# Kernel optimization log

Hardware: AMD Instinct MI355X
Metric: run time of the kernel (lower is better)

## Reference

```python
import jax, jax.numpy as jnp
import numpy as np

B = 16384
A_SCALE = 1.7159
S_SCALE = 2.0 / 3.0
CONNECTIONS = [[0,1,2],[1,2,3],[2,3,4],[3,4,5],[0,4,5],[0,1,5],
               [0,1,2,3],[1,2,3,4],[2,3,4,5],[0,3,4,5],[0,1,4,5],[0,1,2,5],
               [0,1,3,4],[1,2,4,5],[0,2,3,5],[0,1,2,3,4,5]]

def _c3_mask():
    m = np.zeros((16, 6, 1, 1), dtype=np.float32)
    for i, conns in enumerate(CONNECTIONS):
        m[i, conns, 0, 0] = 1.0
    return jnp.asarray(m)

C3_MASK = _c3_mask()

def tanh_act(x):
    return A_SCALE * jnp.tanh(S_SCALE * x)

def conv_valid(x, w):
    # x: (B, Cin, H, W), w: (Cout, Cin, k, k) -> (B, Cout, H-k+1, W-k+1)
    return jax.lax.conv_general_dilated(
        x, w, window_strides=(1, 1), padding='VALID',
        dimension_numbers=('NCHW', 'OIHW', 'NCHW'))

def pool_affine(x, w, b):
    # Faithful to the torch 'efficient' path: reshape(B,C,H/2,W/2,2,2).mean((4,5)).
    # (This is a row-major regrouping, NOT true 2x2 block pooling.)
    bsz, c, h, wd = x.shape
    y = x.reshape(bsz, c, h // 2, wd // 2, 2, 2).mean(axis=(4, 5))
    return w.reshape(1, c, 1, 1) * y + b.reshape(1, c, 1, 1)


def setup_inputs() -> dict:
    key = jax.random.key(0)
    ks = jax.random.split(key, 14)
    inp = {
        'x':     jax.random.normal(ks[0], (B, 1, 32, 32), jnp.float32),
        'w1':    jax.random.normal(ks[1], (6, 1, 5, 5), jnp.float32) * 0.2,
        'b1':    jnp.zeros((6,), jnp.float32),
        's2_w':  jnp.ones((6,), jnp.float32),
        's2_b':  jnp.zeros((6,), jnp.float32),
        'w3':    jax.random.normal(ks[2], (16, 6, 5, 5), jnp.float32) * 0.1,
        'b3':    jnp.zeros((16,), jnp.float32),
        's4_w':  jnp.ones((16,), jnp.float32),
        's4_b':  jnp.zeros((16,), jnp.float32),
        'w5':    jax.random.normal(ks[3], (120, 16, 5, 5), jnp.float32) * 0.05,
        'b5':    jnp.zeros((120,), jnp.float32),
        'f6_w':  jax.random.normal(ks[4], (84, 120), jnp.float32) * 0.09,
        'f6_b':  jnp.zeros((84,), jnp.float32),
        'rbf_w': jax.random.bernoulli(ks[5], 0.3, (10, 84)).astype(jnp.float32),
    }
    return inp


def reference(x, w1, b1, s2_w, s2_b, w3, b3, s4_w, s4_b, w5, b5, f6_w, f6_b, rbf_w):
    # C1: full conv 1->6, per-filter scalar bias
    h = conv_valid(x, w1) + b1.reshape(1, -1, 1, 1)          # (B,6,28,28)
    h = tanh_act(h)
    # S2: avg pool (efficient reshape semantics) + learnable affine
    h = tanh_act(pool_affine(h, s2_w, s2_b))                  # (B,6,14,14)
    # C3: sparsely-connected conv 6->16, implemented as masked full conv
    h = conv_valid(h, w3 * C3_MASK) + b3.reshape(1, -1, 1, 1)  # (B,16,10,10)
    h = tanh_act(h)
    # S4
    h = tanh_act(pool_affine(h, s4_w, s4_b))                  # (B,16,5,5)
    # C5: full conv 16->120 on 5x5 -> 1x1, squeeze to (B,120)
    h = conv_valid(h, w5) + b5.reshape(1, -1, 1, 1)
    h = tanh_act(h.reshape(h.shape[0], 120))                  # (B,120)
    # F6
    h = tanh_act(h @ f6_w.T + f6_b)                           # (B,84)
    # RBF: squared euclidean distance to each class bitmap
    diff = h[:, None, :] - rbf_w[None, :, :]                  # (B,10,84)
    return jnp.sum(diff * diff, axis=2)                       # (B,10)
```

## Files before the change

### kernel.cpp

```cpp
#include <hip/hip_runtime.h>
#include <cstdint>


typedef unsigned int u32;

union U32H2 { u32 u; _Float16 h[2]; };
__device__ __forceinline__ float f16lo(u32 v) { U32H2 a; a.u = v; return (float)a.h[0]; }
__device__ __forceinline__ float f16hi(u32 v) { U32H2 a; a.u = v; return (float)a.h[1]; }
__device__ __forceinline__ u32 packh2(float a, float b) {
    U32H2 x; x.h[0] = (_Float16)a; x.h[1] = (_Float16)b; return x.u;
}

typedef _Float16 h2v __attribute__((ext_vector_type(2)));
union U32V2 { u32 u; h2v v; };

#if defined(__has_builtin)
#if __has_builtin(__builtin_amdgcn_fdot2)
#define HAVE_FDOT2 1
#endif
#endif

__device__ __forceinline__ float dot2(u32 a, u32 b, float c) {
    U32V2 x, y; x.u = a; y.u = b;
#ifdef HAVE_FDOT2
    return __builtin_amdgcn_fdot2(x.v, y.v, c, false);
#else
    return c + (float)x.v[0] * (float)y.v[0] + (float)x.v[1] * (float)y.v[1];
#endif
}

__device__ __forceinline__ float tact(float v) {
    float e = __expf(1.3333333333f * v);
    return 1.7159f * (1.0f - 2.0f * __builtin_amdgcn_rcpf(e + 1.0f));
}

__device__ const int C3_NIC[16] = {3,3,3,3,3,3, 4,4,4,4,4,4,4,4,4, 6};
__device__ const int C3_ICL[96] = {
    0,1,2,0,0,0,  1,2,3,0,0,0,  2,3,4,0,0,0,  3,4,5,0,0,0,
    0,4,5,0,0,0,  0,1,5,0,0,0,  0,1,2,3,0,0,  1,2,3,4,0,0,
    2,3,4,5,0,0,  0,3,4,5,0,0,  0,1,4,5,0,0,  0,1,2,5,0,0,
    0,1,3,4,0,0,  1,2,4,5,0,0,  0,2,3,5,0,0,  0,1,2,3,4,5 };

#define WPK_W1  0
#define WPK_W1S 96
#define WPK_W3  192
#define WPK_W3S 1632
#define WPK_W5  3072
#define WPK_F6  31872
#define WPK_N   36912

__global__ __launch_bounds__(256) void k_wpack(
    const float* __restrict__ w1, const float* __restrict__ w3,
    const float* __restrict__ w5, const float* __restrict__ f6w,
    u32* __restrict__ wpk)
{
    const int idx = blockIdx.x * 256 + threadIdx.x;
    if (idx >= WPK_N) return;
    float a = 0.0f, b = 0.0f;
    if (idx < 192) {
        const int s = idx >= 96;
        const int t = idx - s * 96;
        if (t < 90) {
            int ch = t / 15, r = t % 15, ky = r / 3, q = r % 3;
            const float* w = w1 + ch * 25 + ky * 5;
            if (!s) { a = w[2 * q]; if (q < 2) b = w[2 * q + 1]; }
            else if (q == 0) { b = w[0]; }
            else { a = w[2 * q - 1]; b = w[2 * q]; }
        }
    } else if (idx < WPK_W5) {
        const int s = (idx - WPK_W3) >= 1440;
        const int t = idx - WPK_W3 - s * 1440;
        int p = t / 15, r = t % 15, ky = r / 3, q = r % 3;
        const float* w = w3 + p * 25 + ky * 5;
        if (!s) { a = w[2 * q]; if (q < 2) b = w[2 * q + 1]; }
        else if (q == 0) { b = w[0]; }
        else { a = w[2 * q - 1]; b = w[2 * q]; }
    } else if (idx < WPK_F6) {
        int t = idx - WPK_W5;
        int c = t / 240, r = t % 240, g = r / 3, q = r % 3;
        a = w5[c * 400 + g * 5 + 2 * q];
        if (q < 2) b = w5[c * 400 + g * 5 + 2 * q + 1];
    } else {
        int t = idx - WPK_F6;
        int o = t / 60, i = t % 60;
        a = f6w[o * 120 + 2 * i];
        b = f6w[o * 120 + 2 * i + 1];
    }
    wpk[idx] = packh2(a, b);
}

__global__ __launch_bounds__(256) void k_tr(const float* __restrict__ x,
                                            u32* __restrict__ xp)
{
    __shared__ _Float16 lds[64 * 66];
    const int t = threadIdx.x;
    const int tb = blockIdx.x * 64;
    const int tp = blockIdx.y * 64;
    #pragma unroll
    for (int i = 0; i < 16; ++i) {
        int idx = i * 256 + t;
        int bl = idx >> 6, pl = idx & 63;
        lds[pl * 66 + bl] = (_Float16)x[(size_t)(tb + bl) * 1024 + tp + pl];
    }
    __syncthreads();
    #pragma unroll
    for (int j = 0; j < 8; ++j) {
        int idx = j * 256 + t;
        int pp = idx >> 6, bl = idx & 63;
        U32H2 u;
        u.h[0] = lds[(2 * pp) * 66 + bl];
        u.h[1] = lds[(2 * pp + 1) * 66 + bl];
        xp[(size_t)(blockIdx.y * 32 + pp) * 8192 + tb + bl] = u.u;
    }
}

__global__ __launch_bounds__(256) void k_c1s2(
    const u32* __restrict__ xp, const u32* __restrict__ wpk,
    const float* __restrict__ b1,
    const float* __restrict__ s2w, const float* __restrict__ s2b,
    u32* __restrict__ s2p, int ostr)
{
    const int sl = blockIdx.x * 256 + threadIdx.x;
    const int oy2 = blockIdx.y / 3;
    const int cp  = blockIdx.y % 3;
    const int y0 = 2 * oy2;
    const u32* xb = xp + sl;

    u32 wl[2][15], wls[2][15];
    #pragma unroll
    for (int a = 0; a < 2; ++a) {
        #pragma unroll
        for (int i = 0; i < 15; ++i) wl[a][i]  = wpk[WPK_W1  + (2 * cp + a) * 15 + i];
        #pragma unroll
        for (int i = 0; i < 15; ++i) wls[a][i] = wpk[WPK_W1S + (2 * cp + a) * 15 + i];
    }

    u32 cur[6][4];
    #pragma unroll
    for (int r = 0; r < 6; ++r)
        #pragma unroll
        for (int c = 0; c < 4; ++c)
            cur[r][c] = xb[(size_t)((y0 + r) * 16 + c) * 8192];

    float va[2][7], vb[2][7];

    #pragma unroll
    for (int qx = 0; qx < 7; ++qx) {
        float o[2][2][4];
        #pragma unroll
        for (int a = 0; a < 2; ++a) {
            const float bbv = b1[2 * cp + a];
            #pragma unroll
            for (int u = 0; u < 2; ++u)
                #pragma unroll
                for (int d = 0; d < 4; ++d) o[a][u][d] = bbv;
        }
        #pragma unroll
        for (int r = 0; r < 6; ++r) {
            #pragma unroll
            for (int u = 0; u < 2; ++u) {
                const int ky = r - u;
                if (ky < 0 || ky > 4) continue;
                #pragma unroll
                for (int a = 0; a < 2; ++a) {
                    const u32 w0 = wl[a][ky * 3 + 0];
                    const u32 w1 = wl[a][ky * 3 + 1];
                    const u32 w2 = wl[a][ky * 3 + 2];
                    const u32 v0 = wls[a][ky * 3 + 0];
                    const u32 v1 = wls[a][ky * 3 + 1];
                    const u32 v2 = wls[a][ky * 3 + 2];
                    o[a][u][0] = dot2(cur[r][0], w0, dot2(cur[r][1], w1, dot2(cur[r][2], w2, o[a][u][0])));
                    o[a][u][1] = dot2(cur[r][0], v0, dot2(cur[r][1], v1, dot2(cur[r][2], v2, o[a][u][1])));
                    o[a][u][2] = dot2(cur[r][1], w0, dot2(cur[r][2], w1, dot2(cur[r][3], w2, o[a][u][2])));
                    o[a][u][3] = dot2(cur[r][1], v0, dot2(cur[r][2], v1, dot2(cur[r][3], v2, o[a][u][3])));
                }
            }
        }
        #pragma unroll
        for (int a = 0; a < 2; ++a) {
            const int ch = 2 * cp + a;
            const float sw = s2w[ch], sb = s2b[ch];
            float m0 = 0.25f * (tact(o[a][0][0]) + tact(o[a][0][1]) + tact(o[a][0][2]) + tact(o[a][0][3]));
            float m1 = 0.25f * (tact(o[a][1][0]) + tact(o[a][1][1]) + tact(o[a][1][2]) + tact(o[a][1][3]));
            va[a][qx] = tact(sw * m0 + sb);
            vb[a][qx] = tact(sw * m1 + sb);
        }
        if (qx < 6) {
            #pragma unroll
            for (int r = 0; r < 6; ++r) {
                cur[r][0] = cur[r][2];
                cur[r][1] = cur[r][3];
                cur[r][2] = xb[(size_t)((y0 + r) * 16 + 2 * qx + 4) * 8192];
                cur[r][3] = xb[(size_t)((y0 + r) * 16 + 2 * qx + 5) * 8192];
            }
        }
    }
    #pragma unroll
    for (int a = 0; a < 2; ++a) {
        u32 o7[7];
        o7[0] = packh2(va[a][0], va[a][1]);
        o7[1] = packh2(va[a][2], va[a][3]);
        o7[2] = packh2(va[a][4], va[a][5]);
        o7[3] = packh2(va[a][6], vb[a][0]);
        o7[4] = packh2(vb[a][1], vb[a][2]);
        o7[5] = packh2(vb[a][3], vb[a][4]);
        o7[6] = packh2(vb[a][5], vb[a][6]);
        const int ch = 2 * cp + a;
        const int f0 = ch * 98 + oy2 * 7;
        const int fh0 = f0 >> 1;
        uint2* p2 = (uint2*)s2p;
        uint2 t;
        if ((oy2 & 1) == 0) {
            t.x = o7[0]; t.y = o7[1]; p2[(size_t)(fh0 + 0) * ostr + sl] = t;
            t.x = o7[2]; t.y = o7[3]; p2[(size_t)(fh0 + 1) * ostr + sl] = t;
            t.x = o7[4]; t.y = o7[5]; p2[(size_t)(fh0 + 2) * ostr + sl] = t;
            s2p[((size_t)(fh0 + 3) * ostr + sl) * 2] = o7[6];
        } else {
            s2p[((size_t)fh0 * ostr + sl) * 2 + 1] = o7[0];
            t.x = o7[1]; t.y = o7[2]; p2[(size_t)(fh0 + 1) * ostr + sl] = t;
            t.x = o7[3]; t.y = o7[4]; p2[(size_t)(fh0 + 2) * ostr + sl] = t;
            t.x = o7[5]; t.y = o7[6]; p2[(size_t)(fh0 + 3) * ostr + sl] = t;
        }
    }
}

template<int NIC>
__device__ __forceinline__ void c3_body(
    const uint2* __restrict__ s2c, const u32* __restrict__ wpk,
    const int* __restrict__ icl, int oc, int y2, int nb, int sl,
    float a2[2][10])
{
    #pragma unroll
    for (int e = 0; e < NIC; ++e) {
        const int ic = icl[e];
        const uint2* sp = s2c + (size_t)(ic * 49 + y2 * 7) * nb + sl;
        u32 wa_[6][7];
        #pragma unroll
        for (int k = 0; k < 21; ++k) {
            const uint2 v = sp[(size_t)k * nb];
            wa_[(2 * k) / 7][(2 * k) % 7]         = v.x;
            wa_[(2 * k + 1) / 7][(2 * k + 1) % 7] = v.y;
        }
        u32 wl[15], wls[15];
        #pragma unroll
        for (int i = 0; i < 15; ++i) wl[i]  = wpk[WPK_W3  + (oc * 6 + ic) * 15 + i];
        #pragma unroll
        for (int i = 0; i < 15; ++i) wls[i] = wpk[WPK_W3S + (oc * 6 + ic) * 15 + i];
        #pragma unroll
        for (int r = 0; r < 6; ++r) {
            const u32* wa = wa_[r];
            #pragma unroll
            for (int u = 0; u < 2; ++u) {
                const int ky = r - u;
                if (ky < 0 || ky > 4) continue;
                const u32 w0 = wl[ky * 3 + 0];
                const u32 w1 = wl[ky * 3 + 1];
                const u32 w2 = wl[ky * 3 + 2];
                const u32 v0 = wls[ky * 3 + 0];
                const u32 v1 = wls[ky * 3 + 1];
                const u32 v2 = wls[ky * 3 + 2];
                #pragma unroll
                for (int p = 0; p < 5; ++p) {
                    a2[u][2 * p]     = dot2(wa[p], w0, dot2(wa[p + 1], w1, dot2(wa[p + 2], w2, a2[u][2 * p])));
                    a2[u][2 * p + 1] = dot2(wa[p], v0, dot2(wa[p + 1], v1, dot2(wa[p + 2], v2, a2[u][2 * p + 1])));
                }
            }
        }
    }
}

__global__ __launch_bounds__(256) void k_c3s4(
    const u32* __restrict__ s2p, const u32* __restrict__ wpk,
    const float* __restrict__ b3, const float* __restrict__ s4w,
    const float* __restrict__ s4b, u32* __restrict__ s4p, int nb)
{
    const int sl = blockIdx.x * 256 + threadIdx.x;
    const int oc = blockIdx.y / 5;
    const int y2 = blockIdx.y % 5;
    const uint2* s2c = (const uint2*)s2p;
    const int* icl = &C3_ICL[oc * 6];
    const float bbv = b3[oc];

    float a2[2][10];
    #pragma unroll
    for (int u = 0; u < 2; ++u)
        #pragma unroll
        for (int ox = 0; ox < 10; ++ox) a2[u][ox] = bbv;

    switch (C3_NIC[oc]) {
        case 3:  c3_body<3>(s2c, wpk, icl, oc, y2, nb, sl, a2); break;
        case 4:  c3_body<4>(s2c, wpk, icl, oc, y2, nb, sl, a2); break;
        default: c3_body<6>(s2c, wpk, icl, oc, y2, nb, sl, a2); break;
    }

    float tv[20];
    #pragma unroll
    for (int u = 0; u < 2; ++u)
        #pragma unroll
        for (int ox = 0; ox < 10; ++ox) tv[u * 10 + ox] = tact(a2[u][ox]);
    const float swv = s4w[oc], sbv = s4b[oc];
    float so[5];
    #pragma unroll
    for (int x2 = 0; x2 < 5; ++x2)
        so[x2] = tact(0.25f * (tv[x2 * 4] + tv[x2 * 4 + 1] + tv[x2 * 4 + 2] + tv[x2 * 4 + 3]) * swv + sbv);
    const size_t g = (size_t)(oc * 5 + y2) * 3;
    s4p[(g + 0) * nb + sl] = packh2(so[0], so[1]);
    s4p[(g + 1) * nb + sl] = packh2(so[2], so[3]);
    s4p[(g + 2) * nb + sl] = packh2(so[4], 0.0f);
}

__global__ __launch_bounds__(256) void k_c5(
    const u32* __restrict__ s4p, const u32* __restrict__ wpk,
    const float* __restrict__ b5, u32* __restrict__ h5p, int nb)
{
    const int sl = blockIdx.x * 256 + threadIdx.x;
    const int chg = blockIdx.y;
    const u32* wp = wpk + WPK_W5 + chg * 10 * 240;
    float acc[10];
    #pragma unroll
    for (int c = 0; c < 10; ++c) acc[c] = b5[chg * 10 + c];
    #pragma unroll 4
    for (int i = 0; i < 240; ++i) {
        const u32 v = s4p[(size_t)i * nb + sl];
        #pragma unroll
        for (int c = 0; c < 10; ++c)
            acc[c] = dot2(v, wp[c * 240 + i], acc[c]);
    }
    #pragma unroll
    for (int j = 0; j < 5; ++j)
        h5p[(size_t)(chg * 5 + j) * nb + sl] =
            packh2(tact(acc[2 * j]), tact(acc[2 * j + 1]));
}

__global__ __launch_bounds__(256) void k_f6(
    const u32* __restrict__ h5p, const u32* __restrict__ wpk,
    const float* __restrict__ f6b, u32* __restrict__ h6p, int nb)
{
    const int sl = blockIdx.x * 256 + threadIdx.x;
    const int og = blockIdx.y;
    const u32* wp = wpk + WPK_F6 + og * 14 * 60;
    float acc[14];
    #pragma unroll
    for (int o = 0; o < 14; ++o) acc[o] = f6b[og * 14 + o];
    #pragma unroll 4
    for (int i = 0; i < 60; ++i) {
        const u32 v = h5p[(size_t)i * nb + sl];
        #pragma unroll
        for (int o = 0; o < 14; ++o)
            acc[o] = dot2(v, wp[o * 60 + i], acc[o]);
    }
    #pragma unroll
    for (int j = 0; j < 7; ++j)
        h6p[(size_t)(og * 7 + j) * nb + sl] =
            packh2(tact(acc[2 * j]), tact(acc[2 * j + 1]));
}

__global__ __launch_bounds__(256) void k_rbf(
    const u32* __restrict__ h6p, const float* __restrict__ rbf,
    float* __restrict__ out, int nb)
{
    const int sl = blockIdx.x * 256 + threadIdx.x;
    const int gy = blockIdx.y;
    float hv[84];
    #pragma unroll
    for (int i = 0; i < 42; ++i) {
        const u32 v = h6p[(size_t)i * nb + sl];
        hv[2 * i]     = f16lo(v);
        hv[2 * i + 1] = f16hi(v);
    }
    #pragma unroll
    for (int a = 0; a < 2; ++a) {
        const int c = 2 * gy + a;
        float acc = 0.0f;
        #pragma unroll 4
        for (int i = 0; i < 84; ++i) {
            float d = hv[i] - rbf[c * 84 + i];
            acc += d * d;
        }
        out[(size_t)sl * 10 + c] = acc;
    }
}

extern "C" void kernel_launch(void* const* d_in, const int* in_sizes, int n_in,
                              void* d_out, int out_size, void* d_ws, size_t ws_size,
                              hipStream_t stream)
{
    const float* x    = (const float*)d_in[0];
    const float* w1   = (const float*)d_in[1];
    const float* b1   = (const float*)d_in[2];
    const float* s2w  = (const float*)d_in[3];
    const float* s2b  = (const float*)d_in[4];
    const float* w3   = (const float*)d_in[5];
    const float* b3   = (const float*)d_in[6];
    const float* s4w  = (const float*)d_in[7];
    const float* s4b  = (const float*)d_in[8];
    const float* w5   = (const float*)d_in[9];
    const float* b5   = (const float*)d_in[10];
    const float* f6w  = (const float*)d_in[11];
    const float* f6b  = (const float*)d_in[12];
    const float* rbfw = (const float*)d_in[13];
    float* out = (float*)d_out;
    char* ws = (char*)d_ws;

    u32* WPK = (u32*)((char*)d_out +
                      (((size_t)out_size - (size_t)(WPK_N * 4)) & ~(size_t)7));
    k_wpack<<<dim3((WPK_N + 255) / 256), 256, 0, stream>>>(w1, w3, w5, f6w, WPK);

    if (ws_size >= 55312384) {
        u32* S2P = (u32*)(ws);
        u32* XP  = (u32*)(ws + 38535168);
        u32* S4P = (u32*)(ws + 38535168);
        u32* H5P = (u32*)(ws);
        u32* H6P = (u32*)(ws + 4194304);
        for (int c = 0; c < 2; ++c) {
            k_tr  <<<dim3(128, 16), 256, 0, stream>>>(x + (size_t)c * 8192 * 1024, XP);
            k_c1s2<<<dim3(32, 42), 256, 0, stream>>>(XP, WPK, b1, s2w, s2b,
                                                     S2P + (size_t)c * 16384, 16384);
        }
        k_c3s4<<<dim3(64, 80), 256, 0, stream>>>(S2P, WPK, b3, s4w, s4b, S4P, 16384);
        k_c5  <<<dim3(64, 12), 256, 0, stream>>>(S4P, WPK, b5, H5P, 16384);
        k_f6  <<<dim3(64, 6), 256, 0, stream>>>(H5P, WPK, f6b, H6P, 16384);
        k_rbf <<<dim3(64, 5), 256, 0, stream>>>(H6P, rbfw, out, 16384);
    } else {
        u32* XP  = (u32*)(ws);
        u32* S2P = (u32*)(ws + 16777216);
        u32* S4P = (u32*)(ws);
        u32* H5P = (u32*)(ws + 7864320);
        u32* H6P = (u32*)(ws + 9830400);
        for (int c = 0; c < 2; ++c) {
            k_tr  <<<dim3(128, 16), 256, 0, stream>>>(x + (size_t)c * 8192 * 1024, XP);
            k_c1s2<<<dim3(32, 42), 256, 0, stream>>>(XP, WPK, b1, s2w, s2b, S2P, 8192);
            k_c3s4<<<dim3(32, 80), 256, 0, stream>>>(S2P, WPK, b3, s4w, s4b, S4P, 8192);
            k_c5  <<<dim3(32, 12), 256, 0, stream>>>(S4P, WPK, b5, H5P, 8192);
            k_f6  <<<dim3(32, 6), 256, 0, stream>>>(H5P, WPK, f6b, H6P, 8192);
            k_rbf <<<dim3(32, 5), 256, 0, stream>>>(H6P, rbfw, out + (size_t)c * 8192 * 10, 8192);
        }
    }
}
```

Before: 321.5 us.

## Widen intermediate layouts to 8-byte loads and split C3 into two row halves

All intermediate activation buffers (transposed input, S4, H5, H6) switch from one packed half2 per batch element to uint2 pairs, so each thread issues 8-byte loads and stores. The C3/S4 kernel now computes three or two pooled output rows per block instead of one. This lets a thread reuse one loaded slab of S2 rows across several rows and cuts redundant S2 reads, reducing the grid from 80 to 32 blocks in y. The trade-off is more accumulators and registers per thread, which may lower occupancy, and uneven work between the two halves.

```diff
diff --git a/kernel.cpp b/kernel.cpp
--- a/kernel.cpp
+++ b/kernel.cpp
@@ -104,13 +104,16 @@
     }
     __syncthreads();
     #pragma unroll
-    for (int j = 0; j < 8; ++j) {
+    for (int j = 0; j < 4; ++j) {
         int idx = j * 256 + t;
-        int pp = idx >> 6, bl = idx & 63;
-        U32H2 u;
-        u.h[0] = lds[(2 * pp) * 66 + bl];
-        u.h[1] = lds[(2 * pp + 1) * 66 + bl];
-        xp[(size_t)(blockIdx.y * 32 + pp) * 8192 + tb + bl] = u.u;
+        int pc = idx >> 6, bl = idx & 63;
+        U32H2 u0, u1;
+        u0.h[0] = lds[(4 * pc + 0) * 66 + bl];
+        u0.h[1] = lds[(4 * pc + 1) * 66 + bl];
+        u1.h[0] = lds[(4 * pc + 2) * 66 + bl];
+        u1.h[1] = lds[(4 * pc + 3) * 66 + bl];
+        uint2 o; o.x = u0.u; o.y = u1.u;
+        ((uint2*)xp)[(size_t)(blockIdx.y * 16 + pc) * 8192 + tb + bl] = o;
     }
 }
 
@@ -124,7 +127,7 @@
     const int oy2 = blockIdx.y / 3;
     const int cp  = blockIdx.y % 3;
     const int y0 = 2 * oy2;
-    const u32* xb = xp + sl;
+    const uint2* xb = (const uint2*)xp + sl;
 
     u32 wl[2][15], wls[2][15];
     #pragma unroll
@@ -137,10 +140,13 @@
 
     u32 cur[6][4];
     #pragma unroll
-    for (int r = 0; r < 6; ++r)
-        #pragma unroll
-        for (int c = 0; c < 4; ++c)
-            cur[r][c] = xb[(size_t)((y0 + r) * 16 + c) * 8192];
+    for (int r = 0; r < 6; ++r) {
+        #pragma unroll
+        for (int cc = 0; cc < 2; ++cc) {
+            const uint2 v = xb[(size_t)((y0 + r) * 8 + cc) * 8192];
+            cur[r][2 * cc] = v.x; cur[r][2 * cc + 1] = v.y;
+        }
+    }
 
     float va[2][7], vb[2][7];
 
@@ -188,10 +194,11 @@
         if (qx < 6) {
             #pragma unroll
             for (int r = 0; r < 6; ++r) {
+                const uint2 v = xb[(size_t)((y0 + r) * 8 + qx + 2) * 8192];
                 cur[r][0] = cur[r][2];
                 cur[r][1] = cur[r][3];
-                cur[r][2] = xb[(size_t)((y0 + r) * 16 + 2 * qx + 4) * 8192];
-                cur[r][3] = xb[(size_t)((y0 + r) * 16 + 2 * qx + 5) * 8192];
+                cur[r][2] = v.x;
+                cur[r][3] = v.y;
             }
         }
     }
@@ -224,22 +231,44 @@
     }
 }
 
-template<int NIC>
-__device__ __forceinline__ void c3_body(
+__device__ __forceinline__ void emit_s4(
+    const float a2[2][10], int oc, int y2, float swv, float sbv,
+    u32* __restrict__ s4p, int nb, int sl)
+{
+    float tv[20];
+    #pragma unroll
+    for (int u = 0; u < 2; ++u)
+        #pragma unroll
+        for (int ox = 0; ox < 10; ++ox) tv[u * 10 + ox] = tact(a2[u][ox]);
+    float so[5];
+    #pragma unroll
+    for (int x2 = 0; x2 < 5; ++x2)
+        so[x2] = tact(0.25f * (tv[x2 * 4] + tv[x2 * 4 + 1] + tv[x2 * 4 + 2] + tv[x2 * 4 + 3]) * swv + sbv);
+    const int g0 = (oc * 5 + y2) * 3;
+    #pragma unroll
+    for (int q = 0; q < 3; ++q) {
+        const int g = g0 + q;
+        const float lo = (q < 2) ? so[2 * q] : so[4];
+        const float hi = (q < 2) ? so[2 * q + 1] : 0.0f;
+        s4p[((size_t)(g >> 1) * nb + sl) * 2 + (g & 1)] = packh2(lo, hi);
+    }
+}
+
+template<int NIC, int Y2_0, int NY2, int R0, int NCELL>
+__device__ __forceinline__ void c3_half(
     const uint2* __restrict__ s2c, const u32* __restrict__ wpk,
-    const int* __restrict__ icl, int oc, int y2, int nb, int sl,
-    float a2[2][10])
+    const int* __restrict__ icl, int oc, int nb, int sl,
+    float a2[NY2][2][10])
 {
     #pragma unroll
     for (int e = 0; e < NIC; ++e) {
         const int ic = icl[e];
-        const uint2* sp = s2c + (size_t)(ic * 49 + y2 * 7) * nb + sl;
-        u32 wa_[6][7];
-        #pragma unroll
-        for (int k = 0; k < 21; ++k) {
+        const uint2* sp = s2c + (size_t)(ic * 49 + (R0 * 7) / 2) * nb + sl;
+        u32 wf[NCELL * 2];
+        #pragma unroll
+        for (int k = 0; k < NCELL; ++k) {
             const uint2 v = sp[(size_t)k * nb];
-            wa_[(2 * k) / 7][(2 * k) % 7]         = v.x;
-            wa_[(2 * k + 1) / 7][(2 * k + 1) % 7] = v.y;
+            wf[2 * k] = v.x; wf[2 * k + 1] = v.y;
         }
         u32 wl[15], wls[15];
         #pragma unroll
@@ -247,22 +276,25 @@
         #pragma unroll
         for (int i = 0; i < 15; ++i) wls[i] = wpk[WPK_W3S + (oc * 6 + ic) * 15 + i];
         #pragma unroll
-        for (int r = 0; r < 6; ++r) {
-            const u32* wa = wa_[r];
-            #pragma unroll
-            for (int u = 0; u < 2; ++u) {
-                const int ky = r - u;
-                if (ky < 0 || ky > 4) continue;
-                const u32 w0 = wl[ky * 3 + 0];
-                const u32 w1 = wl[ky * 3 + 1];
-                const u32 w2 = wl[ky * 3 + 2];
-                const u32 v0 = wls[ky * 3 + 0];
-                const u32 v1 = wls[ky * 3 + 1];
-                const u32 v2 = wls[ky * 3 + 2];
+        for (int y = 0; y < NY2; ++y) {
+            #pragma unroll
+            for (int r = 0; r < 6; ++r) {
+                const u32* wa = wf + (2 * (Y2_0 + y) + r - R0) * 7;
                 #pragma unroll
-                for (int p = 0; p < 5; ++p) {
-                    a2[u][2 * p]     = dot2(wa[p], w0, dot2(wa[p + 1], w1, dot2(wa[p + 2], w2, a2[u][2 * p])));
-                    a2[u][2 * p + 1] = dot2(wa[p], v0, dot2(wa[p + 1], v1, dot2(wa[p + 2], v2, a2[u][2 * p + 1])));
+                for (int u = 0; u < 2; ++u) {
+                    const int ky = r - u;
+                    if (ky < 0 || ky > 4) continue;
+                    const u32 w0 = wl[ky * 3 + 0];
+                    const u32 w1 = wl[ky * 3 + 1];
+                    const u32 w2 = wl[ky * 3 + 2];
+                    const u32 v0 = wls[ky * 3 + 0];
+                    const u32 v1 = wls[ky * 3 + 1];
+                    const u32 v2 = wls[ky * 3 + 2];
+                    #pragma unroll
+                    for (int p = 0; p < 5; ++p) {
+                        a2[y][u][2 * p]     = dot2(wa[p], w0, dot2(wa[p + 1], w1, dot2(wa[p + 2], w2, a2[y][u][2 * p])));
+                        a2[y][u][2 * p + 1] = dot2(wa[p], v0, dot2(wa[p + 1], v1, dot2(wa[p + 2], v2, a2[y][u][2 * p + 1])));
+                    }
                 }
             }
         }
@@ -275,38 +307,45 @@
     const float* __restrict__ s4b, u32* __restrict__ s4p, int nb)
 {
     const int sl = blockIdx.x * 256 + threadIdx.x;
-    const int oc = blockIdx.y / 5;
-    const int y2 = blockIdx.y % 5;
+    const int oc = blockIdx.y >> 1;
+    const int hf = blockIdx.y & 1;
     const uint2* s2c = (const uint2*)s2p;
     const int* icl = &C3_ICL[oc * 6];
+    const int nic = C3_NIC[oc];
     const float bbv = b3[oc];
-
-    float a2[2][10];
-    #pragma unroll
-    for (int u = 0; u < 2; ++u)
-        #pragma unroll
-        for (int ox = 0; ox < 10; ++ox) a2[u][ox] = bbv;
-
-    switch (C3_NIC[oc]) {
-        case 3:  c3_body<3>(s2c, wpk, icl, oc, y2, nb, sl, a2); break;
-        case 4:  c3_body<4>(s2c, wpk, icl, oc, y2, nb, sl, a2); break;
-        default: c3_body<6>(s2c, wpk, icl, oc, y2, nb, sl, a2); break;
-    }
-
-    float tv[20];
-    #pragma unroll
-    for (int u = 0; u < 2; ++u)
-        #pragma unroll
-        for (int ox = 0; ox < 10; ++ox) tv[u * 10 + ox] = tact(a2[u][ox]);
     const float swv = s4w[oc], sbv = s4b[oc];
-    float so[5];
-    #pragma unroll
-    for (int x2 = 0; x2 < 5; ++x2)
-        so[x2] = tact(0.25f * (tv[x2 * 4] + tv[x2 * 4 + 1] + tv[x2 * 4 + 2] + tv[x2 * 4 + 3]) * swv + sbv);
-    const size_t g = (size_t)(oc * 5 + y2) * 3;
-    s4p[(g + 0) * nb + sl] = packh2(so[0], so[1]);
-    s4p[(g + 1) * nb + sl] = packh2(so[2], so[3]);
-    s4p[(g + 2) * nb + sl] = packh2(so[4], 0.0f);
+
+    if (hf == 0) {
+        float a2[3][2][10];
+        #pragma unroll
+        for (int y = 0; y < 3; ++y)
+            #pragma unroll
+            for (int u = 0; u < 2; ++u)
+                #pragma unroll
+                for (int ox = 0; ox < 10; ++ox) a2[y][u][ox] = bbv;
+        switch (nic) {
+            case 3:  c3_half<3, 0, 3, 0, 35>(s2c, wpk, icl, oc, nb, sl, a2); break;
+            case 4:  c3_half<4, 0, 3, 0, 35>(s2c, wpk, icl, oc, nb, sl, a2); break;
+            default: c3_half<6, 0, 3, 0, 35>(s2c, wpk, icl, oc, nb, sl, a2); break;
+        }
+        #pragma unroll
+        for (int y = 0; y < 3; ++y) emit_s4(a2[y], oc, y, swv, sbv, s4p, nb, sl);
+    } else {
+        float a2[2][2][10];
+        #pragma unroll
+        for (int y = 0; y < 2; ++y)
+            #pragma unroll
+            for (int u = 0; u < 2; ++u)
+                #pragma unroll
+                for (int ox = 0; ox < 10; ++ox) a2[y][u][ox] = bbv;
+        switch (nic) {
+            case 3:  c3_half<3, 3, 2, 6, 28>(s2c, wpk, icl, oc, nb, sl, a2); break;
+            case 4:  c3_half<4, 3, 2, 6, 28>(s2c, wpk, icl, oc, nb, sl, a2); break;
+            default: c3_half<6, 3, 2, 6, 28>(s2c, wpk, icl, oc, nb, sl, a2); break;
+        }
+        #pragma unroll
+        for (int y = 0; y < 2; ++y) emit_s4(a2[y], oc, 3 + y, swv, sbv, s4p, nb, sl);
+    }
 }
 
 __global__ __launch_bounds__(256) void k_c5(
@@ -315,21 +354,26 @@
 {
     const int sl = blockIdx.x * 256 + threadIdx.x;
     const int chg = blockIdx.y;
-    const u32* wp = wpk + WPK_W5 + chg * 10 * 240;
+    const uint2* sb = (const uint2*)s4p + sl;
+    const u32* wp = wpk + WPK_W5 + chg * 2400;
     float acc[10];
     #pragma unroll
     for (int c = 0; c < 10; ++c) acc[c] = b5[chg * 10 + c];
     #pragma unroll 4
-    for (int i = 0; i < 240; ++i) {
-        const u32 v = s4p[(size_t)i * nb + sl];
-        #pragma unroll
-        for (int c = 0; c < 10; ++c)
-            acc[c] = dot2(v, wp[c * 240 + i], acc[c]);
-    }
-    #pragma unroll
-    for (int j = 0; j < 5; ++j)
-        h5p[(size_t)(chg * 5 + j) * nb + sl] =
+    for (int i = 0; i < 120; ++i) {
+        const uint2 v = sb[(size_t)i * nb];
+        #pragma unroll
+        for (int c = 0; c < 10; ++c) {
+            const u32* w = wp + c * 240 + 2 * i;
+            acc[c] = dot2(v.y, w[1], dot2(v.x, w[0], acc[c]));
+        }
+    }
+    #pragma unroll
+    for (int j = 0; j < 5; ++j) {
+        const int k = chg * 5 + j;
+        h5p[((size_t)(k >> 1) * nb + sl) * 2 + (k & 1)] =
             packh2(tact(acc[2 * j]), tact(acc[2 * j + 1]));
+    }
 }
 
 __global__ __launch_bounds__(256) void k_f6(
@@ -338,21 +382,26 @@
 {
     const int sl = blockIdx.x * 256 + threadIdx.x;
     const int og = blockIdx.y;
+    const uint2* hb = (const uint2*)h5p + sl;
     const u32* wp = wpk + WPK_F6 + og * 14 * 60;
     float acc[14];
     #pragma unroll
     for (int o = 0; o < 14; ++o) acc[o] = f6b[og * 14 + o];
-    #pragma unroll 4
-    for (int i = 0; i < 60; ++i) {
-        const u32 v = h5p[(size_t)i * nb + sl];
-        #pragma unroll
-        for (int o = 0; o < 14; ++o)
-            acc[o] = dot2(v, wp[o * 60 + i], acc[o]);
-    }
-    #pragma unroll
-    for (int j = 0; j < 7; ++j)
-        h6p[(size_t)(og * 7 + j) * nb + sl] =
+    #pragma unroll
+    for (int i = 0; i < 30; ++i) {
+        const uint2 v = hb[(size_t)i * nb];
+        #pragma unroll
+        for (int o = 0; o < 14; ++o) {
+            const u32* w = wp + o * 60 + 2 * i;
+            acc[o] = dot2(v.y, w[1], dot2(v.x, w[0], acc[o]));
+        }
+    }
+    #pragma unroll
+    for (int j = 0; j < 7; ++j) {
+        const int k = og * 7 + j;
+        h6p[((size_t)(k >> 1) * nb + sl) * 2 + (k & 1)] =
             packh2(tact(acc[2 * j]), tact(acc[2 * j + 1]));
+    }
 }
 
 __global__ __launch_bounds__(256) void k_rbf(
@@ -361,12 +410,15 @@
 {
     const int sl = blockIdx.x * 256 + threadIdx.x;
     const int gy = blockIdx.y;
+    const uint2* hb = (const uint2*)h6p + sl;
     float hv[84];
     #pragma unroll
-    for (int i = 0; i < 42; ++i) {
-        const u32 v = h6p[(size_t)i * nb + sl];
-        hv[2 * i]     = f16lo(v);
-        hv[2 * i + 1] = f16hi(v);
+    for (int i = 0; i < 21; ++i) {
+        const uint2 v = hb[(size_t)i * nb];
+        hv[4 * i]     = f16lo(v.x);
+        hv[4 * i + 1] = f16hi(v.x);
+        hv[4 * i + 2] = f16lo(v.y);
+        hv[4 * i + 3] = f16hi(v.y);
     }
     #pragma unroll
     for (int a = 0; a < 2; ++a) {
@@ -417,7 +469,7 @@
             k_c1s2<<<dim3(32, 42), 256, 0, stream>>>(XP, WPK, b1, s2w, s2b,
                                                      S2P + (size_t)c * 16384, 16384);
         }
-        k_c3s4<<<dim3(64, 80), 256, 0, stream>>>(S2P, WPK, b3, s4w, s4b, S4P, 16384);
+        k_c3s4<<<dim3(64, 32), 256, 0, stream>>>(S2P, WPK, b3, s4w, s4b, S4P, 16384);
         k_c5  <<<dim3(64, 12), 256, 0, stream>>>(S4P, WPK, b5, H5P, 16384);
         k_f6  <<<dim3(64, 6), 256, 0, stream>>>(H5P, WPK, f6b, H6P, 16384);
         k_rbf <<<dim3(64, 5), 256, 0, stream>>>(H6P, rbfw, out, 16384);
@@ -430,7 +482,7 @@
         for (int c = 0; c < 2; ++c) {
             k_tr  <<<dim3(128, 16), 256, 0, stream>>>(x + (size_t)c * 8192 * 1024, XP);
             k_c1s2<<<dim3(32, 42), 256, 0, stream>>>(XP, WPK, b1, s2w, s2b, S2P, 8192);
-            k_c3s4<<<dim3(32, 80), 256, 0, stream>>>(S2P, WPK, b3, s4w, s4b, S4P, 8192);
+            k_c3s4<<<dim3(32, 32), 256, 0, stream>>>(S2P, WPK, b3, s4w, s4b, S4P, 8192);
             k_c5  <<<dim3(32, 12), 256, 0, stream>>>(S4P, WPK, b5, H5P, 8192);
             k_f6  <<<dim3(32, 6), 256, 0, stream>>>(H5P, WPK, f6b, H6P, 8192);
             k_rbf <<<dim3(32, 5), 256, 0, stream>>>(H6P, rbfw, out + (size_t)c * 8192 * 10, 8192);
```

After: 333.9 us. +3.9%, slower.

## Rewrite C3+S4 as LDS-staged MFMA GEMM over all output channels

Applied to the files above, without the earlier changes.

Replaces the per-thread fdot2 C3 convolution, which ran one block per output channel and row, with a kernel that stages a 64-sample tile of S2 rows in shared memory. It then computes all 16 output channels at once using 16x16x32 f16 MFMA instructions, with the mask-zeroed weights as the A operand. Each S2 tile is read from global memory once instead of once per output channel. In exchange the kernel uses about 64KB of LDS, does extra work on masked-out connections, and zero-pads K from 90 to 96.

```diff
diff --git a/kernel.cpp b/kernel.cpp
--- a/kernel.cpp
+++ b/kernel.cpp
@@ -12,7 +12,10 @@
 }
 
 typedef _Float16 h2v __attribute__((ext_vector_type(2)));
+typedef _Float16 half8 __attribute__((ext_vector_type(8)));
+typedef float f32x4 __attribute__((ext_vector_type(4)));
 union U32V2 { u32 u; h2v v; };
+union AB8 { u32 u[4]; half8 h; };
 
 #if defined(__has_builtin)
 #if __has_builtin(__builtin_amdgcn_fdot2)
@@ -34,20 +37,17 @@
     return 1.7159f * (1.0f - 2.0f * __builtin_amdgcn_rcpf(e + 1.0f));
 }
 
-__device__ const int C3_NIC[16] = {3,3,3,3,3,3, 4,4,4,4,4,4,4,4,4, 6};
-__device__ const int C3_ICL[96] = {
-    0,1,2,0,0,0,  1,2,3,0,0,0,  2,3,4,0,0,0,  3,4,5,0,0,0,
-    0,4,5,0,0,0,  0,1,5,0,0,0,  0,1,2,3,0,0,  1,2,3,4,0,0,
-    2,3,4,5,0,0,  0,3,4,5,0,0,  0,1,4,5,0,0,  0,1,2,5,0,0,
-    0,1,3,4,0,0,  1,2,4,5,0,0,  0,2,3,5,0,0,  0,1,2,3,4,5 };
+__device__ const u32 C3_MB[16] = {
+    0x07, 0x0E, 0x1C, 0x38, 0x31, 0x23, 0x0F, 0x1E,
+    0x3C, 0x39, 0x33, 0x27, 0x1B, 0x36, 0x2D, 0x3F };
 
 #define WPK_W1  0
 #define WPK_W1S 96
-#define WPK_W3  192
-#define WPK_W3S 1632
-#define WPK_W5  3072
-#define WPK_F6  31872
-#define WPK_N   36912
+#define WPK_W3A 192
+#define WPK_W3S 1728
+#define WPK_W5  3264
+#define WPK_F6  32064
+#define WPK_N   37104
 
 __global__ __launch_bounds__(256) void k_wpack(
     const float* __restrict__ w1, const float* __restrict__ w3,
@@ -68,13 +68,19 @@
             else { a = w[2 * q - 1]; b = w[2 * q]; }
         }
     } else if (idx < WPK_W5) {
-        const int s = (idx - WPK_W3) >= 1440;
-        const int t = idx - WPK_W3 - s * 1440;
-        int p = t / 15, r = t % 15, ky = r / 3, q = r % 3;
-        const float* w = w3 + p * 25 + ky * 5;
-        if (!s) { a = w[2 * q]; if (q < 2) b = w[2 * q + 1]; }
-        else if (q == 0) { b = w[0]; }
-        else { a = w[2 * q - 1]; b = w[2 * q]; }
+        const int t2 = idx - WPK_W3A;
+        const int s = t2 >= 1536;
+        const int t = t2 - s * 1536;
+        const int oc = t / 96, kp = t % 96;
+        if (kp < 90) {
+            int ic = kp / 15, rem = kp % 15, ky = rem / 3, q = rem % 3;
+            if ((C3_MB[oc] >> ic) & 1) {
+                const float* w = w3 + (oc * 6 + ic) * 25 + ky * 5;
+                if (!s) { a = w[2 * q]; if (q < 2) b = w[2 * q + 1]; }
+                else if (q == 0) { b = w[0]; }
+                else { a = w[2 * q - 1]; b = w[2 * q]; }
+            }
+        }
     } else if (idx < WPK_F6) {
         int t = idx - WPK_W5;
         int c = t / 240, r = t % 240, g = r / 3, q = r % 3;
@@ -224,89 +230,120 @@
     }
 }
 
-template<int NIC>
-__device__ __forceinline__ void c3_body(
-    const uint2* __restrict__ s2c, const u32* __restrict__ wpk,
-    const int* __restrict__ icl, int oc, int y2, int nb, int sl,
-    float a2[2][10])
-{
-    #pragma unroll
-    for (int e = 0; e < NIC; ++e) {
-        const int ic = icl[e];
-        const uint2* sp = s2c + (size_t)(ic * 49 + y2 * 7) * nb + sl;
-        u32 wa_[6][7];
-        #pragma unroll
-        for (int k = 0; k < 21; ++k) {
-            const uint2 v = sp[(size_t)k * nb];
-            wa_[(2 * k) / 7][(2 * k) % 7]         = v.x;
-            wa_[(2 * k + 1) / 7][(2 * k + 1) % 7] = v.y;
-        }
-        u32 wl[15], wls[15];
-        #pragma unroll
-        for (int i = 0; i < 15; ++i) wl[i]  = wpk[WPK_W3  + (oc * 6 + ic) * 15 + i];
-        #pragma unroll
-        for (int i = 0; i < 15; ++i) wls[i] = wpk[WPK_W3S + (oc * 6 + ic) * 15 + i];
-        #pragma unroll
-        for (int r = 0; r < 6; ++r) {
-            const u32* wa = wa_[r];
-            #pragma unroll
-            for (int u = 0; u < 2; ++u) {
-                const int ky = r - u;
-                if (ky < 0 || ky > 4) continue;
-                const u32 w0 = wl[ky * 3 + 0];
-                const u32 w1 = wl[ky * 3 + 1];
-                const u32 w2 = wl[ky * 3 + 2];
-                const u32 v0 = wls[ky * 3 + 0];
-                const u32 v1 = wls[ky * 3 + 1];
-                const u32 v2 = wls[ky * 3 + 2];
-                #pragma unroll
-                for (int p = 0; p < 5; ++p) {
-                    a2[u][2 * p]     = dot2(wa[p], w0, dot2(wa[p + 1], w1, dot2(wa[p + 2], w2, a2[u][2 * p])));
-                    a2[u][2 * p + 1] = dot2(wa[p], v0, dot2(wa[p + 1], v1, dot2(wa[p + 2], v2, a2[u][2 * p + 1])));
-                }
-            }
-        }
-    }
-}
-
-__global__ __launch_bounds__(256) void k_c3s4(
+__global__ __launch_bounds__(256) void k_c3s4m(
     const u32* __restrict__ s2p, const u32* __restrict__ wpk,
     const float* __restrict__ b3, const float* __restrict__ s4w,
     const float* __restrict__ s4b, u32* __restrict__ s4p, int nb)
 {
-    const int sl = blockIdx.x * 256 + threadIdx.x;
-    const int oc = blockIdx.y / 5;
-    const int y2 = blockIdx.y % 5;
+    __shared__ u32 lds[252 * 65];
+    const int t = threadIdx.x;
+    const int y2 = blockIdx.y;
+    const int base = blockIdx.x * 64;
     const uint2* s2c = (const uint2*)s2p;
-    const int* icl = &C3_ICL[oc * 6];
-    const float bbv = b3[oc];
-
-    float a2[2][10];
-    #pragma unroll
-    for (int u = 0; u < 2; ++u)
-        #pragma unroll
-        for (int ox = 0; ox < 10; ++ox) a2[u][ox] = bbv;
-
-    switch (C3_NIC[oc]) {
-        case 3:  c3_body<3>(s2c, wpk, icl, oc, y2, nb, sl, a2); break;
-        case 4:  c3_body<4>(s2c, wpk, icl, oc, y2, nb, sl, a2); break;
-        default: c3_body<6>(s2c, wpk, icl, oc, y2, nb, sl, a2); break;
-    }
-
-    float tv[20];
-    #pragma unroll
-    for (int u = 0; u < 2; ++u)
-        #pragma unroll
-        for (int ox = 0; ox < 10; ++ox) tv[u * 10 + ox] = tact(a2[u][ox]);
-    const float swv = s4w[oc], sbv = s4b[oc];
-    float so[5];
-    #pragma unroll
-    for (int x2 = 0; x2 < 5; ++x2)
-        so[x2] = tact(0.25f * (tv[x2 * 4] + tv[x2 * 4 + 1] + tv[x2 * 4 + 2] + tv[x2 * 4 + 3]) * swv + sbv);
-    const size_t g = (size_t)(oc * 5 + y2) * 3;
-    s4p[(g + 0) * nb + sl] = packh2(so[0], so[1]);
-    s4p[(g + 1) * nb + sl] = packh2(so[2], so[3]);
-    s4p[(g + 2) * nb + sl] = packh2(so[4], 0.0f);
+
+    for (int i = 0; i < 32; ++i) {
+        int idx = i * 256 + t;
+        if (idx < 8064) {
+            int ic = idx / 1344;
+            int r = idx - ic * 1344;
+            int cell = r >> 6, sLoc = r & 63;
+            uint2 v = s2c[(size_t)(49 * ic + 7 * y2 + cell) * nb + base + sLoc];
+            lds[(ic * 42 + 2 * cell) * 65 + sLoc]     = v.x;
+            lds[(ic * 42 + 2 * cell + 1) * 65 + sLoc] = v.y;
+        }
+    }
+
+    const int l = t & 63, w = t >> 6;
+    const int g = l >> 4, col = l & 15;
+    const int sLocal = w * 16 + col;
+    const int ocA = col;
+
+    AB8 wA[6], wS[6];
+    #pragma unroll
+    for (int s = 0; s < 6; ++s)
+        #pragma unroll
+        for (int m = 0; m < 4; ++m) {
+            int kp = 16 * s + 4 * g + m;
+            wA[s].u[m] = wpk[WPK_W3A + ocA * 96 + kp];
+            wS[s].u[m] = wpk[WPK_W3S + ocA * 96 + kp];
+        }
+
+    int vbase[6][4];
+    u32 zmask[4];
+    #pragma unroll
+    for (int s = 0; s < 6; ++s)
+        #pragma unroll
+        for (int m = 0; m < 4; ++m) {
+            int kp = 16 * s + 4 * g + m;
+            int ic = kp / 15;
+            int rem = kp - ic * 15;
+            int kr = rem / 3;
+            int pr = rem - kr * 3;
+            int c = ic * 42 + kr * 7 + pr;
+            if (kp >= 90) c = 240;
+            vbase[s][m] = c * 65 + sLocal;
+            if (s == 5) zmask[m] = (kp < 90) ? 0xFFFFFFFFu : 0u;
+        }
+
+    float b3v[4], swv[4], sbv[4];
+    #pragma unroll
+    for (int r = 0; r < 4; ++r) {
+        b3v[r] = b3[4 * g + r];
+        swv[r] = s4w[4 * g + r];
+        sbv[r] = s4b[4 * g + r];
+    }
+
+    __syncthreads();
+
+    float pool[4][5];
+    #pragma unroll
+    for (int r = 0; r < 4; ++r)
+        #pragma unroll
+        for (int x2 = 0; x2 < 5; ++x2) pool[r][x2] = 0.0f;
+
+    #pragma unroll
+    for (int q = 0; q < 5; ++q) {
+        f32x4 a00 = {0.f, 0.f, 0.f, 0.f};
+        f32x4 a01 = {0.f, 0.f, 0.f, 0.f};
+        f32x4 a10 = {0.f, 0.f, 0.f, 0.f};
+        f32x4 a11 = {0.f, 0.f, 0.f, 0.f};
+        #pragma unroll
+        for (int s = 0; s < 6; ++s) {
+            AB8 b0, b1;
+            #pragma unroll
+            for (int m = 0; m < 4; ++m) {
+                u32 x0 = lds[vbase[s][m] + q * 65];
+                u32 x1 = lds[vbase[s][m] + (q + 7) * 65];
+                if (s == 5) { x0 &= zmask[m]; x1 &= zmask[m]; }
+                b0.u[m] = x0; b1.u[m] = x1;
+            }
+            a00 = __builtin_amdgcn_mfma_f32_16x16x32_f16(wA[s].h, b0.h, a00, 0, 0, 0);
+            a01 = __builtin_amdgcn_mfma_f32_16x16x32_f16(wS[s].h, b0.h, a01, 0, 0, 0);
+            a10 = __builtin_amdgcn_mfma_f32_16x16x32_f16(wA[s].h, b1.h, a10, 0, 0, 0);
+            a11 = __builtin_amdgcn_mfma_f32_16x16x32_f16(wS[s].h, b1.h, a11, 0, 0, 0);
+        }
+        #pragma unroll
+        for (int r = 0; r < 4; ++r) {
+            pool[r][(2 * q) >> 2]      += tact(a00[r] + b3v[r]);
+            pool[r][(2 * q + 1) >> 2]  += tact(a01[r] + b3v[r]);
+            pool[r][(10 + 2 * q) >> 2] += tact(a10[r] + b3v[r]);
+            pool[r][(11 + 2 * q) >> 2] += tact(a11[r] + b3v[r]);
+        }
+    }
+
+    const int sG = base + sLocal;
+    #pragma unroll
+    for (int r = 0; r < 4; ++r) {
+        float so[5];
+        #pragma unroll
+        for (int x2 = 0; x2 < 5; ++x2)
+            so[x2] = tact(0.25f * pool[r][x2] * swv[r] + sbv[r]);
+        const int ocr = 4 * g + r;
+        const size_t gf = (size_t)(ocr * 5 + y2) * 3;
+        s4p[(gf + 0) * nb + sG] = packh2(so[0], so[1]);
+        s4p[(gf + 1) * nb + sG] = packh2(so[2], so[3]);
+        s4p[(gf + 2) * nb + sG] = packh2(so[4], 0.0f);
+    }
 }
 
 __global__ __launch_bounds__(256) void k_c5(
@@ -417,7 +454,7 @@
             k_c1s2<<<dim3(32, 42), 256, 0, stream>>>(XP, WPK, b1, s2w, s2b,
                                                      S2P + (size_t)c * 16384, 16384);
         }
-        k_c3s4<<<dim3(64, 80), 256, 0, stream>>>(S2P, WPK, b3, s4w, s4b, S4P, 16384);
+        k_c3s4m<<<dim3(256, 5), 256, 0, stream>>>(S2P, WPK, b3, s4w, s4b, S4P, 16384);
         k_c5  <<<dim3(64, 12), 256, 0, stream>>>(S4P, WPK, b5, H5P, 16384);
         k_f6  <<<dim3(64, 6), 256, 0, stream>>>(H5P, WPK, f6b, H6P, 16384);
         k_rbf <<<dim3(64, 5), 256, 0, stream>>>(H6P, rbfw, out, 16384);
@@ -430,7 +467,7 @@
         for (int c = 0; c < 2; ++c) {
             k_tr  <<<dim3(128, 16), 256, 0, stream>>>(x + (size_t)c * 8192 * 1024, XP);
             k_c1s2<<<dim3(32, 42), 256, 0, stream>>>(XP, WPK, b1, s2w, s2b, S2P, 8192);
-            k_c3s4<<<dim3(32, 80), 256, 0, stream>>>(S2P, WPK, b3, s4w, s4b, S4P, 8192);
+            k_c3s4m<<<dim3(128, 5), 256, 0, stream>>>(S2P, WPK, b3, s4w, s4b, S4P, 8192);
             k_c5  <<<dim3(32, 12), 256, 0, stream>>>(S4P, WPK, b5, H5P, 8192);
             k_f6  <<<dim3(32, 6), 256, 0, stream>>>(H5P, WPK, f6b, H6P, 8192);
             k_rbf <<<dim3(32, 5), 256, 0, stream>>>(H6P, rbfw, out + (size_t)c * 8192 * 10, 8192);
```

New measurement: 315.6 us. Within noise of the previous version (-1.9%).
